# Optimization experiments

Hardware: AMD Instinct MI355X
Metric: run time of the kernel (lower is better)

Reference implementation:

```python
import jax, jax.numpy as jnp
import numpy as np

D = 1024
N_HEAD = 16
D_HEAD = D // N_HEAD


def setup_inputs() -> dict:
    key = jax.random.key(0)
    k1, k2, k3 = jax.random.split(key, 3)
    x = jax.random.normal(k1, (4, 2048, D), dtype=jnp.float32)
    # torch nn.Linear weights: [out_features, in_features]
    W_qkv = jax.random.normal(k2, (3 * D, D), dtype=jnp.float32) * (1.0 / np.sqrt(D))
    W_o = jax.random.normal(k3, (D, D), dtype=jnp.float32) * (1.0 / np.sqrt(D))
    return {"x": x, "W_qkv": W_qkv, "W_o": W_o}


def reference(x, W_qkv, W_o):
    b, s, d = x.shape
    qkv = x @ W_qkv.T                      # [b, s, 3d]
    q, k, v = jnp.split(qkv, 3, axis=-1)
    # [b, s, d] -> [b, h, s, dh]
    def heads(z):
        return z.reshape(b, s, N_HEAD, D_HEAD).transpose(0, 2, 1, 3)
    q, k, v = heads(q), heads(k), heads(v)
    scores = jnp.einsum("bhqd,bhkd->bhqk", q, k) / np.sqrt(D_HEAD).astype(np.float32)
    causal = jnp.tril(jnp.ones((s, s), dtype=bool))  # True = keep
    scores = jnp.where(causal, scores, -jnp.inf)
    attn = jax.nn.softmax(scores, axis=-1)
    out = jnp.einsum("bhqk,bhkd->bhqd", attn, v)     # [b, h, s, dh]
    out = out.transpose(0, 2, 1, 3).reshape(b, s, d)
    return out @ W_o.T
```

## Files before the change

### kernel.cpp

```cpp
#include <hip/hip_runtime.h>


typedef _Float16 f16x8 __attribute__((ext_vector_type(8)));
typedef float floatx4 __attribute__((ext_vector_type(4)));
typedef unsigned int uint2v __attribute__((ext_vector_type(2)));

union U4H8 { uint4 u; f16x8 h; };

__device__ __forceinline__ ushort f32_to_h_bits(float f) {
  _Float16 h = (_Float16)f;
  return __builtin_bit_cast(ushort, h);
}
__device__ __forceinline__ uint pack2h(float a, float b) {
  return (uint)f32_to_h_bits(a) | ((uint)f32_to_h_bits(b) << 16);
}
__device__ __forceinline__ float exp2_fast(float x) {
  float r;
  asm("v_exp_f32 %0, %1" : "=v"(r) : "v"(x));
  return r;
}

__device__ __forceinline__ void gld16(const void* g, void* l) {
  __builtin_amdgcn_global_load_lds(
      (const __attribute__((address_space(1))) unsigned char*)g,
      (__attribute__((address_space(3))) unsigned char*)l, 16, 0, 0);
}

__global__ __launch_bounds__(256) void cast_f32_f16(const float* __restrict__ in,
                                                    ushort* __restrict__ out) {
  int i = blockIdx.x * 256 + threadIdx.x;
  float4 v = ((const float4*)in)[i];
  ushort4 o;
  o.x = f32_to_h_bits(v.x);
  o.y = f32_to_h_bits(v.y);
  o.z = f32_to_h_bits(v.z);
  o.w = f32_to_h_bits(v.w);
  ((ushort4*)out)[i] = o;
}

template <int OUT_F16>
__global__ __launch_bounds__(256) void gemm_bt(const ushort* __restrict__ A,
                                               const ushort* __restrict__ B,
                                               void* __restrict__ Cv,
                                               int M, int N, int K) {
  __shared__ ushort As[3][4096];
  __shared__ ushort Bs[3][4096];

  const int tid = threadIdx.x;
  const int lane = tid & 63;
  const int w = tid >> 6;
  const int l15 = lane & 15;
  const int quad = lane >> 4;

  const int gx = gridDim.x;
  const int lin = blockIdx.y * gx + blockIdx.x;
  const int qq = (gx * gridDim.y) >> 3;
  const int nl = (lin & 7) * qq + (lin >> 3);
  const int m0 = (nl / gx) * 128;
  const int n0 = (nl % gx) * 128;

  const int wm = (w & 1) * 64;
  const int wn = (w >> 1) * 64;

  floatx4 acc[4][4];
#pragma unroll
  for (int i = 0; i < 4; i++)
#pragma unroll
    for (int j = 0; j < 4; j++) acc[i][j] = (floatx4){0.f, 0.f, 0.f, 0.f};

  const int srow = w * 16 + (lane >> 2);
  const int sq = ((lane & 3) ^ ((lane >> 3) & 3)) * 8;
  const ushort* Ap = A + (size_t)(m0 + srow) * K + sq;
  const ushort* Bp = B + (size_t)(n0 + srow) * K + sq;
  const size_t rstep = (size_t)64 * K;

  auto stage = [&](int k0, int buf) {
    gld16(Ap + k0, &As[buf][w * 512]);
    gld16(Ap + rstep + k0, &As[buf][(w + 4) * 512]);
    gld16(Bp + k0, &Bs[buf][w * 512]);
    gld16(Bp + rstep + k0, &Bs[buf][(w + 4) * 512]);
  };

  stage(0, 0);
  stage(32, 1);

  const int psw = (quad ^ ((l15 >> 1) & 3)) * 8;

  int bt = 0;
  int bs = 2;
  for (int k0 = 0; k0 < K; k0 += 32) {
    if (k0 + 64 < K) {
      asm volatile("s_waitcnt vmcnt(4)" ::: "memory");
    } else {
      asm volatile("s_waitcnt vmcnt(0)" ::: "memory");
    }
    __builtin_amdgcn_s_barrier();
    asm volatile("" ::: "memory");
    if (k0 + 64 < K) stage(k0 + 64, bs);

    U4H8 af[4], bf[4];
#pragma unroll
    for (int mi = 0; mi < 4; mi++)
      af[mi].u = *(const uint4*)&As[bt][(wm + mi * 16 + l15) * 32 + psw];
#pragma unroll
    for (int ni = 0; ni < 4; ni++)
      bf[ni].u = *(const uint4*)&Bs[bt][(wn + ni * 16 + l15) * 32 + psw];
#pragma unroll
    for (int mi = 0; mi < 4; mi++)
#pragma unroll
      for (int ni = 0; ni < 4; ni++)
        acc[mi][ni] = __builtin_amdgcn_mfma_f32_16x16x32_f16(af[mi].h, bf[ni].h,
                                                             acc[mi][ni], 0, 0, 0);
    bt = (bt == 2) ? 0 : bt + 1;
    bs = (bs == 2) ? 0 : bs + 1;
  }

#pragma unroll
  for (int mi = 0; mi < 4; mi++) {
#pragma unroll
    for (int r = 0; r < 4; r++) {
      size_t row = m0 + wm + mi * 16 + quad * 4 + r;
#pragma unroll
      for (int ni = 0; ni < 4; ni++) {
        size_t col = n0 + wn + ni * 16 + l15;
        float v = acc[mi][ni][r];
        if (OUT_F16)
          ((ushort*)Cv)[row * N + col] = f32_to_h_bits(v);
        else
          ((float*)Cv)[row * N + col] = v;
      }
    }
  }
}

__global__ __launch_bounds__(256) void vtrans(const ushort* __restrict__ qkv,
                                              ushort* __restrict__ vtg) {
  __shared__ ushort T[64 * 66];
  const int tid = threadIdx.x;
  const int kt = blockIdx.x;
  const int bh = blockIdx.y;
  const int b = bh >> 4, h = bh & 15;

  const int r = tid >> 3;
  const int c = (tid & 7) * 8;
  const ushort* src = qkv + (size_t)(b * 2048 + kt * 64) * 3072 + 2048 + h * 64;
  uint4 v0 = *(const uint4*)(src + (size_t)r * 3072 + c);
  uint4 v1 = *(const uint4*)(src + (size_t)(r + 32) * 3072 + c);
  union { uint4 u; ushort s[8]; } a0, a1;
  a0.u = v0; a1.u = v1;
#pragma unroll
  for (int j = 0; j < 8; j++) {
    T[(c + j) * 66 + r] = a0.s[j];
    T[(c + j) * 66 + r + 32] = a1.s[j];
  }
  __syncthreads();

  const int d = tid >> 3;
  const int kc = (tid & 7) * 8;
  ushort* dst = vtg + (size_t)bh * 64 * 2048 + (size_t)kt * 64;
  union { uint u[4]; uint4 u4; } o0, o1;
#pragma unroll
  for (int i = 0; i < 4; i++) {
    o0.u[i] = *(const uint*)&T[d * 66 + kc + 2 * i];
    o1.u[i] = *(const uint*)&T[(d + 32) * 66 + kc + 2 * i];
  }
  *(uint4*)(dst + (size_t)d * 2048 + kc) = o0.u4;
  *(uint4*)(dst + (size_t)(d + 32) * 2048 + kc) = o1.u4;
}

__global__ __launch_bounds__(256, 4) void attn_fused(const ushort* __restrict__ qkv,
                                                     const ushort* __restrict__ vtg,
                                                     ushort* __restrict__ attn_out) {
  __shared__ ushort Ks[2][4096];
  __shared__ ushort Vs[2][4096];
  __shared__ ushort Ps[4][16 * 40];

  const int tid = threadIdx.x;
  const int lane = tid & 63;
  const int w = tid >> 6;
  const int l15 = lane & 15;
  const int quad = lane >> 4;
  const int id = blockIdx.x;
  const int n_ = id >> 3;
  const int bx = n_ >> 3;
  const int bh = (id & 7) * 8 + (n_ & 7);
  const int b = bh >> 4;
  const int h = bh & 15;
  const int bS = b * 2048;
  const int qtA = bx;
  const int qtB = 31 - bx;
  const int ktmax = qtB;
  int q0s[2];
  q0s[0] = qtA * 64 + w * 16;
  q0s[1] = qtB * 64 + w * 16;

  U4H8 qf[2][2];
#pragma unroll
  for (int s = 0; s < 2; s++) {
    const ushort* qrow = qkv + (size_t)(bS + q0s[s] + l15) * 3072 + h * 64;
#pragma unroll
    for (int kc = 0; kc < 2; kc++) {
      qf[s][kc].u = *(const uint4*)(qrow + kc * 32 + quad * 8);
      qf[s][kc].h = qf[s][kc].h * (_Float16)0.1803368787f;
    }
  }

  floatx4 o[2][4];
#pragma unroll
  for (int s = 0; s < 2; s++)
#pragma unroll
    for (int ni = 0; ni < 4; ni++) o[s][ni] = (floatx4){0.f, 0.f, 0.f, 0.f};
  float m_i[2] = {-1e30f, -1e30f}, l_i[2] = {0.f, 0.f};

  const ushort* kbase = qkv + (size_t)bS * 3072 + 1024 + h * 64;
  const ushort* vbase = vtg + (size_t)bh * 64 * 2048;
  const int sr = lane & 15;
  const int scc = (lane >> 4) * 8;

  auto stage = [&](int kt, int buf) {
    const ushort* kg = kbase + (size_t)(kt * 64 + w * 16 + sr) * 3072 + scc;
    gld16(kg, &Ks[buf][(w * 2 + 0) * 512]);
    gld16(kg + 32, &Ks[buf][(w * 2 + 1) * 512]);
    const ushort* vg = vbase + (size_t)(w * 16 + sr) * 2048 + (size_t)kt * 64 + scc;
    gld16(vg, &Vs[buf][(w * 2 + 0) * 512]);
    gld16(vg + 32, &Vs[buf][(w * 2 + 1) * 512]);
  };

  auto strip_step = [&](int s, bool diag, int kt64, int buf) {
    floatx4 s4[4];
    __builtin_amdgcn_s_setprio(1);
#pragma unroll
    for (int t = 0; t < 4; t++) {
      U4H8 kf0, kf1;
      kf0.u = *(const uint4*)&Ks[buf][(t * 2 + 0) * 512 + lane * 8];
      kf1.u = *(const uint4*)&Ks[buf][(t * 2 + 1) * 512 + lane * 8];
      floatx4 sa = (floatx4){0.f, 0.f, 0.f, 0.f};
      sa = __builtin_amdgcn_mfma_f32_16x16x32_f16(kf0.h, qf[s][0].h, sa, 0, 0, 0);
      sa = __builtin_amdgcn_mfma_f32_16x16x32_f16(kf1.h, qf[s][1].h, sa, 0, 0, 0);
      s4[t] = sa;
    }
    __builtin_amdgcn_s_setprio(0);
    if (diag) {
      const int q = q0s[s] + l15;
#pragma unroll
      for (int t = 0; t < 4; t++)
#pragma unroll
        for (int r = 0; r < 4; r++) {
          int key = kt64 + t * 16 + quad * 4 + r;
          if (key > q) s4[t][r] = -1e30f;
        }
    }

    float tmax = -1e30f;
#pragma unroll
    for (int t = 0; t < 4; t++)
#pragma unroll
      for (int r = 0; r < 4; r++) tmax = fmaxf(tmax, s4[t][r]);
    tmax = fmaxf(tmax, __shfl_xor(tmax, 16));
    tmax = fmaxf(tmax, __shfl_xor(tmax, 32));
    if (__any(tmax > m_i[s])) {
      float mnew = fmaxf(m_i[s], tmax);
      float alpha = exp2_fast(m_i[s] - mnew);
      m_i[s] = mnew;
      l_i[s] *= alpha;
#pragma unroll
      for (int ni = 0; ni < 4; ni++) o[s][ni] *= alpha;
    }
    const float m2 = m_i[s];
    float rs = 0.f;
#pragma unroll
    for (int t = 0; t < 4; t++)
#pragma unroll
      for (int r = 0; r < 4; r++) {
        float p = exp2_fast(s4[t][r] - m2);
        s4[t][r] = p;
        rs += p;
      }
    rs += __shfl_xor(rs, 16);
    rs += __shfl_xor(rs, 32);
    l_i[s] += rs;

#pragma unroll
    for (int kc = 0; kc < 2; kc++) {
      uint pA = pack2h(s4[kc * 2][0], s4[kc * 2][1]);
      uint pB = pack2h(s4[kc * 2][2], s4[kc * 2][3]);
      uint pC = pack2h(s4[kc * 2 + 1][0], s4[kc * 2 + 1][1]);
      uint pD = pack2h(s4[kc * 2 + 1][2], s4[kc * 2 + 1][3]);
      uint2v ac = __builtin_amdgcn_permlane32_swap(pA, pC, false, false);
      uint2v bd = __builtin_amdgcn_permlane32_swap(pB, pD, false, false);
      uint2v ac2 = __builtin_amdgcn_permlane16_swap(ac[0], ac[1], false, false);
      uint2v bd2 = __builtin_amdgcn_permlane16_swap(bd[0], bd[1], false, false);
      U4H8 pb;
      pb.u = (uint4){ac2[0], bd2[0], ac2[1], bd2[1]};
      __builtin_amdgcn_s_setprio(1);
#pragma unroll
      for (int ni = 0; ni < 4; ni++) {
        U4H8 vf;
        vf.u = *(const uint4*)&Vs[buf][(ni * 2 + kc) * 512 + lane * 8];
        o[s][ni] = __builtin_amdgcn_mfma_f32_16x16x32_f16(vf.h, pb.h, o[s][ni], 0, 0, 0);
      }
      __builtin_amdgcn_s_setprio(0);
    }
  };

  stage(0, 0);
  for (int kt = 0; kt <= ktmax; ++kt) {
    const int buf = kt & 1;
    __syncthreads();
    if (kt < ktmax) stage(kt + 1, buf ^ 1);
    strip_step(1, kt == qtB, kt * 64, buf);
    if (kt <= qtA) strip_step(0, kt == qtA, kt * 64, buf);
  }

#pragma unroll
  for (int s = 0; s < 2; s++) {
    float inv = 1.0f / l_i[s];
    ushort* orow = attn_out + (size_t)(bS + q0s[s] + l15) * 1024 + h * 64;
#pragma unroll
    for (int p = 0; p < 2; p++) {
#pragma unroll
      for (int nh = 0; nh < 2; nh++) {
        const int ni = p * 2 + nh;
        *(uint*)&Ps[w][l15 * 40 + nh * 16 + quad * 4] =
            pack2h(o[s][ni][0] * inv, o[s][ni][1] * inv);
        *(uint*)&Ps[w][l15 * 40 + nh * 16 + quad * 4 + 2] =
            pack2h(o[s][ni][2] * inv, o[s][ni][3] * inv);
      }
      __asm__ volatile("s_waitcnt lgkmcnt(0)" ::: "memory");
      uint4 x = *(const uint4*)&Ps[w][l15 * 40 + quad * 8];
      *(uint4*)(orow + p * 32 + quad * 8) = x;
      __asm__ volatile("s_waitcnt lgkmcnt(0)" ::: "memory");
    }
  }
}

extern "C" void kernel_launch(void* const* d_in, const int* in_sizes, int n_in,
                              void* d_out, int out_size, void* d_ws, size_t ws_size,
                              hipStream_t stream) {
  const float* x = (const float*)d_in[0];
  const float* wqkv = (const float*)d_in[1];
  const float* wo = (const float*)d_in[2];
  float* out = (float*)d_out;

  ushort* xh = (ushort*)d_ws;
  ushort* wqkvh = xh + (size_t)8192 * 1024;
  ushort* woh = wqkvh + (size_t)3072 * 1024;
  ushort* qkvh = woh + (size_t)1024 * 1024;
  ushort* attnh = qkvh + (size_t)8192 * 3072;
  ushort* vtg = attnh + (size_t)8192 * 1024;

  cast_f32_f16<<<8192, 256, 0, stream>>>(x, xh);
  cast_f32_f16<<<3072, 256, 0, stream>>>(wqkv, wqkvh);
  cast_f32_f16<<<1024, 256, 0, stream>>>(wo, woh);

  gemm_bt<1><<<dim3(24, 64), 256, 0, stream>>>(xh, wqkvh, qkvh, 8192, 3072, 1024);
  vtrans<<<dim3(32, 64), 256, 0, stream>>>(qkvh, vtg);
  attn_fused<<<dim3(1024), 256, 0, stream>>>(qkvh, vtg, attnh);
  gemm_bt<0><<<dim3(8, 64), 256, 0, stream>>>(attnh, woh, out, 8192, 1024, 1024);
}
```

Measured before the change: 257.2 us.

## Interleave both query strips per key tile and drop LDS epilogue staging

On key tiles shared by both query strips, the attention loop now does the QK^T MFMAs, softmax and PV MFMAs for both strips together. This gives the scheduler two independent MFMA chains and lets each K and V fragment read from LDS be used twice. Probabilities are packed to fp16 with the round-toward-zero cvt_pkrtz instead of per-element conversion. The output epilogue uses permlane swaps instead of an LDS round trip with waitcnts. The risks are higher register pressure at 4 waves per SIMD and slightly different rounding of P.

```diff
diff --git a/kernel.cpp b/kernel.cpp
--- a/kernel.cpp
+++ b/kernel.cpp
@@ -2,6 +2,7 @@
 
 
 typedef _Float16 f16x8 __attribute__((ext_vector_type(8)));
+typedef __fp16 fp16x2 __attribute__((ext_vector_type(2)));
 typedef float floatx4 __attribute__((ext_vector_type(4)));
 typedef unsigned int uint2v __attribute__((ext_vector_type(2)));
 
@@ -13,11 +14,23 @@
 }
 __device__ __forceinline__ uint pack2h(float a, float b) {
   return (uint)f32_to_h_bits(a) | ((uint)f32_to_h_bits(b) << 16);
+}
+__device__ __forceinline__ uint pkrtz(float a, float b) {
+  fp16x2 r = __builtin_amdgcn_cvt_pkrtz(a, b);
+  return __builtin_bit_cast(uint, r);
 }
 __device__ __forceinline__ float exp2_fast(float x) {
   float r;
   asm("v_exp_f32 %0, %1" : "=v"(r) : "v"(x));
   return r;
+}
+
+__device__ __forceinline__ uint4 qtrans(uint pA, uint pB, uint pC, uint pD) {
+  uint2v ac = __builtin_amdgcn_permlane32_swap(pA, pC, false, false);
+  uint2v bd = __builtin_amdgcn_permlane32_swap(pB, pD, false, false);
+  uint2v ac2 = __builtin_amdgcn_permlane16_swap(ac[0], ac[1], false, false);
+  uint2v bd2 = __builtin_amdgcn_permlane16_swap(bd[0], bd[1], false, false);
+  return (uint4){ac2[0], bd2[0], ac2[1], bd2[1]};
 }
 
 __device__ __forceinline__ void gld16(const void* g, void* l) {
@@ -173,7 +186,6 @@
                                                      ushort* __restrict__ attn_out) {
   __shared__ ushort Ks[2][4096];
   __shared__ ushort Vs[2][4096];
-  __shared__ ushort Ps[4][16 * 40];
 
   const int tid = threadIdx.x;
   const int lane = tid & 63;
@@ -226,38 +238,17 @@
     gld16(vg + 32, &Vs[buf][(w * 2 + 1) * 512]);
   };
 
-  auto strip_step = [&](int s, bool diag, int kt64, int buf) {
-    floatx4 s4[4];
-    __builtin_amdgcn_s_setprio(1);
-#pragma unroll
-    for (int t = 0; t < 4; t++) {
-      U4H8 kf0, kf1;
-      kf0.u = *(const uint4*)&Ks[buf][(t * 2 + 0) * 512 + lane * 8];
-      kf1.u = *(const uint4*)&Ks[buf][(t * 2 + 1) * 512 + lane * 8];
-      floatx4 sa = (floatx4){0.f, 0.f, 0.f, 0.f};
-      sa = __builtin_amdgcn_mfma_f32_16x16x32_f16(kf0.h, qf[s][0].h, sa, 0, 0, 0);
-      sa = __builtin_amdgcn_mfma_f32_16x16x32_f16(kf1.h, qf[s][1].h, sa, 0, 0, 0);
-      s4[t] = sa;
-    }
-    __builtin_amdgcn_s_setprio(0);
-    if (diag) {
-      const int q = q0s[s] + l15;
-#pragma unroll
-      for (int t = 0; t < 4; t++)
-#pragma unroll
-        for (int r = 0; r < 4; r++) {
-          int key = kt64 + t * 16 + quad * 4 + r;
-          if (key > q) s4[t][r] = -1e30f;
-        }
-    }
-
-    float tmax = -1e30f;
-#pragma unroll
-    for (int t = 0; t < 4; t++)
-#pragma unroll
-      for (int r = 0; r < 4; r++) tmax = fmaxf(tmax, s4[t][r]);
-    tmax = fmaxf(tmax, __shfl_xor(tmax, 16));
-    tmax = fmaxf(tmax, __shfl_xor(tmax, 32));
+  auto redmax = [&](const floatx4* ss) {
+    float a = fmaxf(fmaxf(ss[0][0], ss[0][1]), fmaxf(ss[0][2], ss[0][3]));
+    float b2 = fmaxf(fmaxf(ss[1][0], ss[1][1]), fmaxf(ss[1][2], ss[1][3]));
+    float c = fmaxf(fmaxf(ss[2][0], ss[2][1]), fmaxf(ss[2][2], ss[2][3]));
+    float d = fmaxf(fmaxf(ss[3][0], ss[3][1]), fmaxf(ss[3][2], ss[3][3]));
+    float t = fmaxf(fmaxf(a, b2), fmaxf(c, d));
+    t = fmaxf(t, __shfl_xor(t, 16));
+    t = fmaxf(t, __shfl_xor(t, 32));
+    return t;
+  };
+  auto resc = [&](int s, float tmax) {
     if (__any(tmax > m_i[s])) {
       float mnew = fmaxf(m_i[s], tmax);
       float alpha = exp2_fast(m_i[s] - mnew);
@@ -266,38 +257,121 @@
 #pragma unroll
       for (int ni = 0; ni < 4; ni++) o[s][ni] *= alpha;
     }
-    const float m2 = m_i[s];
+  };
+  auto expsum = [&](floatx4* ss, float m2) {
     float rs = 0.f;
 #pragma unroll
     for (int t = 0; t < 4; t++)
 #pragma unroll
       for (int r = 0; r < 4; r++) {
-        float p = exp2_fast(s4[t][r] - m2);
-        s4[t][r] = p;
+        float p = exp2_fast(ss[t][r] - m2);
+        ss[t][r] = p;
         rs += p;
       }
+    return rs;
+  };
+  auto qsum = [&](float rs) {
     rs += __shfl_xor(rs, 16);
     rs += __shfl_xor(rs, 32);
-    l_i[s] += rs;
+    return rs;
+  };
+  auto mask = [&](floatx4* ss, int s, int kt64) {
+    const int q = q0s[s] + l15;
+#pragma unroll
+    for (int t = 0; t < 4; t++)
+#pragma unroll
+      for (int r = 0; r < 4; r++) {
+        int key = kt64 + t * 16 + quad * 4 + r;
+        if (key > q) ss[t][r] = -1e30f;
+      }
+  };
+  auto ptrans = [&](const floatx4* ss, int kc) {
+    return qtrans(pkrtz(ss[kc * 2][0], ss[kc * 2][1]),
+                  pkrtz(ss[kc * 2][2], ss[kc * 2][3]),
+                  pkrtz(ss[kc * 2 + 1][0], ss[kc * 2 + 1][1]),
+                  pkrtz(ss[kc * 2 + 1][2], ss[kc * 2 + 1][3]));
+  };
+
+  auto step_dual = [&](bool diag0, int kt64, int buf) {
+    floatx4 s1[4], s0[4];
+    __builtin_amdgcn_s_setprio(1);
+#pragma unroll
+    for (int t = 0; t < 4; t++) {
+      U4H8 kf0, kf1;
+      kf0.u = *(const uint4*)&Ks[buf][(t * 2 + 0) * 512 + lane * 8];
+      kf1.u = *(const uint4*)&Ks[buf][(t * 2 + 1) * 512 + lane * 8];
+      floatx4 a = (floatx4){0.f, 0.f, 0.f, 0.f};
+      floatx4 b2 = (floatx4){0.f, 0.f, 0.f, 0.f};
+      a = __builtin_amdgcn_mfma_f32_16x16x32_f16(kf0.h, qf[1][0].h, a, 0, 0, 0);
+      b2 = __builtin_amdgcn_mfma_f32_16x16x32_f16(kf0.h, qf[0][0].h, b2, 0, 0, 0);
+      a = __builtin_amdgcn_mfma_f32_16x16x32_f16(kf1.h, qf[1][1].h, a, 0, 0, 0);
+      b2 = __builtin_amdgcn_mfma_f32_16x16x32_f16(kf1.h, qf[0][1].h, b2, 0, 0, 0);
+      s1[t] = a;
+      s0[t] = b2;
+    }
+    __builtin_amdgcn_s_setprio(0);
+    if (diag0) mask(s0, 0, kt64);
+
+    float t1 = redmax(s1);
+    float t0 = redmax(s0);
+    resc(1, t1);
+    resc(0, t0);
+    float rs1 = expsum(s1, m_i[1]);
+    float rs0 = expsum(s0, m_i[0]);
+    rs1 = qsum(rs1);
+    rs0 = qsum(rs0);
+    l_i[1] += rs1;
+    l_i[0] += rs0;
 
 #pragma unroll
     for (int kc = 0; kc < 2; kc++) {
-      uint pA = pack2h(s4[kc * 2][0], s4[kc * 2][1]);
-      uint pB = pack2h(s4[kc * 2][2], s4[kc * 2][3]);
-      uint pC = pack2h(s4[kc * 2 + 1][0], s4[kc * 2 + 1][1]);
-      uint pD = pack2h(s4[kc * 2 + 1][2], s4[kc * 2 + 1][3]);
-      uint2v ac = __builtin_amdgcn_permlane32_swap(pA, pC, false, false);
-      uint2v bd = __builtin_amdgcn_permlane32_swap(pB, pD, false, false);
-      uint2v ac2 = __builtin_amdgcn_permlane16_swap(ac[0], ac[1], false, false);
-      uint2v bd2 = __builtin_amdgcn_permlane16_swap(bd[0], bd[1], false, false);
-      U4H8 pb;
-      pb.u = (uint4){ac2[0], bd2[0], ac2[1], bd2[1]};
+      U4H8 b1, b0;
+      b1.u = ptrans(s1, kc);
+      b0.u = ptrans(s0, kc);
       __builtin_amdgcn_s_setprio(1);
 #pragma unroll
       for (int ni = 0; ni < 4; ni++) {
         U4H8 vf;
         vf.u = *(const uint4*)&Vs[buf][(ni * 2 + kc) * 512 + lane * 8];
-        o[s][ni] = __builtin_amdgcn_mfma_f32_16x16x32_f16(vf.h, pb.h, o[s][ni], 0, 0, 0);
+        o[1][ni] = __builtin_amdgcn_mfma_f32_16x16x32_f16(vf.h, b1.h, o[1][ni], 0, 0, 0);
+        o[0][ni] = __builtin_amdgcn_mfma_f32_16x16x32_f16(vf.h, b0.h, o[0][ni], 0, 0, 0);
+      }
+      __builtin_amdgcn_s_setprio(0);
+    }
+  };
+
+  auto step_single = [&](bool diag1, int kt64, int buf) {
+    floatx4 s1[4];
+    __builtin_amdgcn_s_setprio(1);
+#pragma unroll
+    for (int t = 0; t < 4; t++) {
+      U4H8 kf0, kf1;
+      kf0.u = *(const uint4*)&Ks[buf][(t * 2 + 0) * 512 + lane * 8];
+      kf1.u = *(const uint4*)&Ks[buf][(t * 2 + 1) * 512 + lane * 8];
+      floatx4 a = (floatx4){0.f, 0.f, 0.f, 0.f};
+      a = __builtin_amdgcn_mfma_f32_16x16x32_f16(kf0.h, qf[1][0].h, a, 0, 0, 0);
+      a = __builtin_amdgcn_mfma_f32_16x16x32_f16(kf1.h, qf[1][1].h, a, 0, 0, 0);
+      s1[t] = a;
+    }
+    __builtin_amdgcn_s_setprio(0);
+    if (diag1) mask(s1, 1, kt64);
+
+    float t1 = redmax(s1);
+    resc(1, t1);
+    float rs1 = expsum(s1, m_i[1]);
+    rs1 = qsum(rs1);
+    l_i[1] += rs1;
+
+#pragma unroll
+    for (int kc = 0; kc < 2; kc++) {
+      U4H8 b1;
+      b1.u = ptrans(s1, kc);
+      __builtin_amdgcn_s_setprio(1);
+#pragma unroll
+      for (int ni = 0; ni < 4; ni++) {
+        U4H8 vf;
+        vf.u = *(const uint4*)&Vs[buf][(ni * 2 + kc) * 512 + lane * 8];
+        o[1][ni] = __builtin_amdgcn_mfma_f32_16x16x32_f16(vf.h, b1.h, o[1][ni], 0, 0, 0);
       }
       __builtin_amdgcn_s_setprio(0);
     }
@@ -308,8 +382,8 @@
     const int buf = kt & 1;
     __syncthreads();
     if (kt < ktmax) stage(kt + 1, buf ^ 1);
-    strip_step(1, kt == qtB, kt * 64, buf);
-    if (kt <= qtA) strip_step(0, kt == qtA, kt * 64, buf);
+    if (kt <= qtA) step_dual(kt == qtA, kt * 64, buf);
+    else step_single(kt == qtB, kt * 64, buf);
   }
 
 #pragma unroll
@@ -318,18 +392,11 @@
     ushort* orow = attn_out + (size_t)(bS + q0s[s] + l15) * 1024 + h * 64;
 #pragma unroll
     for (int p = 0; p < 2; p++) {
-#pragma unroll
-      for (int nh = 0; nh < 2; nh++) {
-        const int ni = p * 2 + nh;
-        *(uint*)&Ps[w][l15 * 40 + nh * 16 + quad * 4] =
-            pack2h(o[s][ni][0] * inv, o[s][ni][1] * inv);
-        *(uint*)&Ps[w][l15 * 40 + nh * 16 + quad * 4 + 2] =
-            pack2h(o[s][ni][2] * inv, o[s][ni][3] * inv);
-      }
-      __asm__ volatile("s_waitcnt lgkmcnt(0)" ::: "memory");
-      uint4 x = *(const uint4*)&Ps[w][l15 * 40 + quad * 8];
+      uint4 x = qtrans(pack2h(o[s][p * 2][0] * inv, o[s][p * 2][1] * inv),
+                       pack2h(o[s][p * 2][2] * inv, o[s][p * 2][3] * inv),
+                       pack2h(o[s][p * 2 + 1][0] * inv, o[s][p * 2 + 1][1] * inv),
+                       pack2h(o[s][p * 2 + 1][2] * inv, o[s][p * 2 + 1][3] * inv));
       *(uint4*)(orow + p * 32 + quad * 8) = x;
-      __asm__ volatile("s_waitcnt lgkmcnt(0)" ::: "memory");
     }
   }
 }
```

Measured after the change: 300.5 us. +16.8%, slower.
